# Performance work log

Hardware: AMD Instinct MI355X
Metric: run time of the kernel (lower is better)

The kernel has to match this reference:

```python
import jax, jax.numpy as jnp
import numpy as np

B, L, H, D_IN = 64, 4096, 128, 3

def setup_inputs() -> dict:
    key = jax.random.key(0)
    ks = jax.random.split(key, 9)
    def lin_w(k, fan_in, shape):
        bound = 1.0 / np.sqrt(fan_in)
        return jax.random.uniform(k, shape, jnp.float32, -bound, bound)
    return {
        "x": jax.random.normal(ks[0], (B, L, D_IN), jnp.float32),
        "Wp": lin_w(ks[1], D_IN, (D_IN, H)), "bp": lin_w(ks[2], D_IN, (H,)),
        "Wz": lin_w(ks[3], H, (H, H)),      "bz": lin_w(ks[4], H, (H,)),
        "Wh": lin_w(ks[5], H, (H, H)),      "bh": lin_w(ks[6], H, (H,)),
        "Wg": lin_w(ks[7], H, (H, 1)),      "bg": lin_w(ks[8], H, (1,)),
    }

def reference(x, Wp, bp, Wz, bz, Wh, bh, Wg, bg):
    # Batched projections across all timesteps (B, L, H)
    inp = x @ Wp + bp                      # input_proj
    z = jax.nn.sigmoid(inp @ Wz + bz)      # update gate
    h_tilde = jnp.tanh(inp @ Wh + bh)      # candidate
    # Linear recurrence h_t = a_t * h_{t-1} + b_t, h_{-1} = 0
    a = 1.0 - z
    b = z * h_tilde
    def combine(c1, c2):
        a1, b1 = c1
        a2, b2 = c2
        return (a1 * a2, b1 * a2 + b2)
    _, h = jax.lax.associative_scan(combine, (a, b), axis=1)  # h_t (since h_{-1}=0)
    # Readout uses h BEFORE the update at each step: preds_t = gauss_head(h_{t-1})
    h_prev = jnp.concatenate([jnp.zeros_like(h[:, :1]), h[:, :-1]], axis=1)
    preds = h_prev @ Wg + bg               # (B, L, 1)
    return preds
```

## Files before the change

### kernel.cpp

```cpp
#include <hip/hip_runtime.h>
#include <hip/hip_bf16.h>
#include <stdint.h>

#define B_   64
#define L_   4096
#define H_   128
#define HG_  32
#define NG_  4
#define TI_  256
#define NIT_ 16
#define PADI 136

typedef __attribute__((ext_vector_type(8))) short short8;
typedef __attribute__((ext_vector_type(4))) short short4v;
typedef __attribute__((ext_vector_type(4))) float floatx4;
typedef __attribute__((ext_vector_type(2))) float floatx2;

#define LOG2E 1.44269504088896340736f

__device__ __forceinline__ unsigned short f2bf(float f){
    unsigned int u = __float_as_uint(f);
    u += 0x7FFFu + ((u >> 16) & 1u);
    return (unsigned short)(u >> 16);
}
__device__ __forceinline__ float bf2f(unsigned short s){
    return __uint_as_float(((unsigned int)s) << 16);
}

__global__ void prep_w(const float* __restrict__ Wz, const float* __restrict__ Wh,
                       unsigned short* __restrict__ WzT, unsigned short* __restrict__ WhT){
    int b = blockIdx.x;
    const float* W = (b < 16) ? Wz : Wh;
    unsigned short* WT = (b < 16) ? WzT : WhT;
    int b16 = b & 15, tid = threadIdx.x;
    #pragma unroll
    for (int it = 0; it < 4; ++it){
        int idx = b16*1024 + it*256 + tid;
        int n = idx >> 7, k = idx & 127;
        WT[idx] = f2bf(W[k*H_ + n]);
    }
}

__global__ __launch_bounds__(1024, 4)
void fused_rnn(const float* __restrict__ x,
               const float* __restrict__ Wp, const float* __restrict__ bp,
               const float* __restrict__ bz, const float* __restrict__ bh,
               const float* __restrict__ Wg,
               const unsigned short* __restrict__ WzT,
               const unsigned short* __restrict__ WhT,
               float* __restrict__ partials)
{
    __shared__ __align__(16) unsigned short s_inp[TI_*PADI];
    __shared__ __align__(16) unsigned int  s_ab[TI_*HG_];
    __shared__ __align__(16) floatx2 s_agg[32*32];
    __shared__ float s_hh[32*32];

    const int bid = blockIdx.x;
    const int bb  = bid >> 2;
    const int g   = bid & 3;
    const int tid = threadIdx.x;
    const int wv = tid >> 6, lane = tid & 63, quad = lane >> 4, l15 = lane & 15;

    const int G   = wv >> 3;
    const int tt0 = wv & 7;
    const int sh  = tid & 31;
    const int ss  = tid >> 5;
    const int rh  = tid >> 5;
    const int rs  = tid & 31;
    const int cg  = tid & 31;
    const int tg  = tid >> 5;
    const int rt  = tid >> 2;
    const int rp  = tid & 3;

    const unsigned short* WT = G ? WhT : WzT;
    short8 bfr[2][4];
    #pragma unroll
    for (int ct = 0; ct < 2; ++ct)
        #pragma unroll
        for (int kk = 0; kk < 4; ++kk)
            bfr[ct][kk] = *(const short8*)&WT[(g*HG_ + ct*16 + l15)*H_ + kk*32 + quad*8];
    float biasv[2];
    #pragma unroll
    for (int ct = 0; ct < 2; ++ct)
        biasv[ct] = (G ? bh : bz)[g*HG_ + ct*16 + l15];
    const float wgv = Wg[g*HG_ + sh];
    float w0[4], w1[4], w2[4], bc[4];
    #pragma unroll
    for (int m = 0; m < 4; ++m){
        w0[m] = Wp[cg*4+m]; w1[m] = Wp[H_+cg*4+m]; w2[m] = Wp[2*H_+cg*4+m];
        bc[m] = bp[cg*4+m];
    }
    float h_run = 0.0f;

    for (int it = 0; it < NIT_; ++it){
        if (it > 0){
            float s = 0.0f;
            #pragma unroll
            for (int i = 0; i < 8; ++i){
                int col = rp*8 + i;
                s += ((const float*)s_ab)[rt*HG_ + (col ^ (rt & 31))];
            }
            s += __shfl_xor(s, 1);
            s += __shfl_xor(s, 2);
            if (rp == 0)
                partials[(((size_t)(g*B_ + bb)) << 12) + (it-1)*TI_ + rt] = s;
        }
        {
            const float* xr0 = x + ((size_t)bb*L_ + it*TI_ + tg*8)*3;
            #pragma unroll
            for (int j = 0; j < 8; ++j){
                int t = tg*8 + j;
                float x0 = xr0[j*3], x1 = xr0[j*3+1], x2 = xr0[j*3+2];
                short4v pk;
                #pragma unroll
                for (int m = 0; m < 4; ++m){
                    float v = bc[m];
                    v = fmaf(x0, w0[m], v);
                    v = fmaf(x1, w1[m], v);
                    v = fmaf(x2, w2[m], v);
                    pk[m] = (short)f2bf(v);
                }
                *(short4v*)&s_inp[t*PADI + cg*4] = pk;
            }
        }
        __syncthreads();

        #pragma unroll
        for (int tl = 0; tl < 2; ++tl){
            int tile = tt0 + tl*8;
            floatx4 acc0 = (floatx4){0.f,0.f,0.f,0.f};
            floatx4 acc1 = (floatx4){0.f,0.f,0.f,0.f};
            #pragma unroll
            for (int kk = 0; kk < 4; ++kk){
                short8 af = *(const short8*)&s_inp[(tile*16 + l15)*PADI + kk*32 + quad*8];
                acc0 = __builtin_amdgcn_mfma_f32_16x16x32_bf16(af, bfr[0][kk], acc0, 0, 0, 0);
                acc1 = __builtin_amdgcn_mfma_f32_16x16x32_bf16(af, bfr[1][kk], acc1, 0, 0, 0);
            }
            #pragma unroll
            for (int ct = 0; ct < 2; ++ct){
                floatx4 acc = ct ? acc1 : acc0;
                int hl = ct*16 + l15;
                #pragma unroll
                for (int e = 0; e < 4; ++e){
                    int t = tile*16 + quad*4 + e;
                    float v = acc[e] + biasv[ct];
                    float r;
                    if (G == 0){
                        r = __builtin_amdgcn_rcpf(1.0f + __builtin_amdgcn_exp2f(v * LOG2E));
                    } else {
                        float ex = __builtin_amdgcn_exp2f(2.0f*LOG2E*v);
                        r = 1.0f - 2.0f*__builtin_amdgcn_rcpf(ex + 1.0f);
                    }
                    ((unsigned short*)s_ab)[(t*HG_ + (hl ^ (t & 31)))*2 + G] = f2bf(r);
                }
            }
        }
        __syncthreads();

        float aj[8], bj[8];
        {
            float A = 1.0f, Q = 0.0f;
            #pragma unroll
            for (int j = 0; j < 8; ++j){
                int t = ss*8 + j;
                unsigned int u = s_ab[t*HG_ + (sh ^ (t & 31))];
                float a  = bf2f((unsigned short)(u & 0xffffu));
                float th = bf2f((unsigned short)(u >> 16));
                float b  = fmaf(-a, th, th);
                aj[j] = a; bj[j] = b;
                Q = fmaf(a, Q, b);
                A *= a;
            }
            s_agg[ss*32 + (sh ^ ss)] = (floatx2){A, Q};
        }
        __syncthreads();

        {
            floatx2 v = s_agg[rs*32 + (rh ^ rs)];
            float P = v[0], Hq = v[1];
            #pragma unroll
            for (int d = 1; d < 32; d <<= 1){
                float pP = __shfl_up(P, d, 32);
                float pH = __shfl_up(Hq, d, 32);
                if (rs >= d){
                    Hq = fmaf(P, pH, Hq);
                    P  = P * pP;
                }
            }
            float eP = __shfl_up(P, 1, 32);
            float eH = __shfl_up(Hq, 1, 32);
            if (rs == 0){ eP = 1.0f; eH = 0.0f; }
            float tP = __shfl(P, 31, 32);
            float tH = __shfl(Hq, 31, 32);
            s_hh[rs*32 + (rh ^ rs)] = fmaf(eP, h_run, eH);
            h_run = fmaf(tP, h_run, tH);
        }
        __syncthreads();

        {
            float hh = s_hh[ss*32 + (sh ^ ss)];
            #pragma unroll
            for (int j = 0; j < 8; ++j){
                int t = ss*8 + j;
                ((float*)s_ab)[t*HG_ + (sh ^ (t & 31))] = wgv * hh;
                hh = fmaf(aj[j], hh, bj[j]);
            }
        }
        __syncthreads();
    }

    {
        float s = 0.0f;
        #pragma unroll
        for (int i = 0; i < 8; ++i){
            int col = rp*8 + i;
            s += ((const float*)s_ab)[rt*HG_ + (col ^ (rt & 31))];
        }
        s += __shfl_xor(s, 1);
        s += __shfl_xor(s, 2);
        if (rp == 0)
            partials[(((size_t)(g*B_ + bb)) << 12) + (NIT_-1)*TI_ + rt] = s;
    }
}

__global__ __launch_bounds__(1024)
void gather(const float* __restrict__ partials, const float* __restrict__ bg,
            float* __restrict__ preds)
{
    size_t idx = (size_t)blockIdx.x*1024 + threadIdx.x;
    const size_t GSTRIDE = (size_t)B_ * L_;
    float s = bg[0];
    s += partials[idx];
    s += partials[GSTRIDE + idx];
    s += partials[2*GSTRIDE + idx];
    s += partials[3*GSTRIDE + idx];
    preds[idx] = s;
}

extern "C" void kernel_launch(void* const* d_in, const int* in_sizes, int n_in,
                              void* d_out, int out_size, void* d_ws, size_t ws_size,
                              hipStream_t stream){
    const float* x  = (const float*)d_in[0];
    const float* Wp = (const float*)d_in[1];
    const float* bp = (const float*)d_in[2];
    const float* Wz = (const float*)d_in[3];
    const float* bz = (const float*)d_in[4];
    const float* Wh = (const float*)d_in[5];
    const float* bh = (const float*)d_in[6];
    const float* Wg = (const float*)d_in[7];
    const float* bg = (const float*)d_in[8];
    float* preds = (float*)d_out;

    uint8_t* w8 = (uint8_t*)d_ws;
    unsigned short* WzT = (unsigned short*)(w8);
    unsigned short* WhT = (unsigned short*)(w8 + 32768);
    float* partials = (float*)(w8 + 65536);

    hipLaunchKernelGGL(prep_w, dim3(32), dim3(256), 0, stream, Wz, Wh, WzT, WhT);
    hipLaunchKernelGGL(fused_rnn, dim3(B_*NG_), dim3(1024), 0, stream,
                       x, Wp, bp, bz, bh, Wg, WzT, WhT, partials);
    hipLaunchKernelGGL(gather, dim3(B_*L_/1024), dim3(1024), 0, stream,
                       partials, bg, preds);
}
```

Measured before the change: 153.0 us.

## Fold weight prep into main kernel, prefetch x, and reduce readout via shuffles

```diff
diff --git a/kernel.cpp b/kernel.cpp
--- a/kernel.cpp
+++ b/kernel.cpp
@@ -10,9 +10,9 @@
 #define TI_  256
 #define NIT_ 16
 #define PADI 136
+#define SW(t) ((((t) << 2) ^ (t)) & 31)
 
 typedef __attribute__((ext_vector_type(8))) short short8;
-typedef __attribute__((ext_vector_type(4))) short short4v;
 typedef __attribute__((ext_vector_type(4))) float floatx4;
 typedef __attribute__((ext_vector_type(2))) float floatx2;
 
@@ -26,28 +26,17 @@
 __device__ __forceinline__ float bf2f(unsigned short s){
     return __uint_as_float(((unsigned int)s) << 16);
 }
-
-__global__ void prep_w(const float* __restrict__ Wz, const float* __restrict__ Wh,
-                       unsigned short* __restrict__ WzT, unsigned short* __restrict__ WhT){
-    int b = blockIdx.x;
-    const float* W = (b < 16) ? Wz : Wh;
-    unsigned short* WT = (b < 16) ? WzT : WhT;
-    int b16 = b & 15, tid = threadIdx.x;
-    #pragma unroll
-    for (int it = 0; it < 4; ++it){
-        int idx = b16*1024 + it*256 + tid;
-        int n = idx >> 7, k = idx & 127;
-        WT[idx] = f2bf(W[k*H_ + n]);
-    }
+__device__ __forceinline__ unsigned int pack2(float lo, float hi){
+    __hip_bfloat162 h = __float22bfloat162_rn(make_float2(lo, hi));
+    return *reinterpret_cast<unsigned int*>(&h);
 }
 
 __global__ __launch_bounds__(1024, 4)
 void fused_rnn(const float* __restrict__ x,
                const float* __restrict__ Wp, const float* __restrict__ bp,
-               const float* __restrict__ bz, const float* __restrict__ bh,
+               const float* __restrict__ Wz, const float* __restrict__ bz,
+               const float* __restrict__ Wh, const float* __restrict__ bh,
                const float* __restrict__ Wg,
-               const unsigned short* __restrict__ WzT,
-               const unsigned short* __restrict__ WhT,
                float* __restrict__ partials)
 {
     __shared__ __align__(16) unsigned short s_inp[TI_*PADI];
@@ -69,16 +58,34 @@
     const int rs  = tid & 31;
     const int cg  = tid & 31;
     const int tg  = tid >> 5;
-    const int rt  = tid >> 2;
-    const int rp  = tid & 3;
-
-    const unsigned short* WT = G ? WhT : WzT;
+
+    {
+        unsigned short* s_w = s_inp;
+        const int gate = tid >> 9;
+        const int r    = tid & 511;
+        const int k    = r >> 2;
+        const int nn0  = (r & 3) * 8;
+        const float* Wsrc = gate ? Wh : Wz;
+        const float* p = Wsrc + (size_t)k*H_ + g*HG_ + nn0;
+        floatx4 a = *(const floatx4*)p;
+        floatx4 b = *(const floatx4*)(p + 4);
+        #pragma unroll
+        for (int j = 0; j < 4; ++j){
+            s_w[gate*4096 + (nn0+j)*H_ + k]   = f2bf(a[j]);
+            s_w[gate*4096 + (nn0+4+j)*H_ + k] = f2bf(b[j]);
+        }
+    }
+    __syncthreads();
+
     short8 bfr[2][4];
-    #pragma unroll
-    for (int ct = 0; ct < 2; ++ct)
+    {
+        const unsigned short* wbase = s_inp + G*4096;
         #pragma unroll
-        for (int kk = 0; kk < 4; ++kk)
-            bfr[ct][kk] = *(const short8*)&WT[(g*HG_ + ct*16 + l15)*H_ + kk*32 + quad*8];
+        for (int ct = 0; ct < 2; ++ct)
+            #pragma unroll
+            for (int kk = 0; kk < 4; ++kk)
+                bfr[ct][kk] = *(const short8*)&wbase[(ct*16 + l15)*H_ + kk*32 + quad*8];
+    }
     float biasv[2];
     #pragma unroll
     for (int ct = 0; ct < 2; ++ct)
@@ -91,36 +98,36 @@
         bc[m] = bp[cg*4+m];
     }
     float h_run = 0.0f;
+    __syncthreads();
+
+    const float* xbase = x + ((size_t)bb*L_ + tg*8)*3;
+    floatx4 xr[6];
+    #pragma unroll
+    for (int q = 0; q < 6; ++q) xr[q] = *(const floatx4*)(xbase + q*4);
 
     for (int it = 0; it < NIT_; ++it){
-        if (it > 0){
-            float s = 0.0f;
-            #pragma unroll
-            for (int i = 0; i < 8; ++i){
-                int col = rp*8 + i;
-                s += ((const float*)s_ab)[rt*HG_ + (col ^ (rt & 31))];
-            }
-            s += __shfl_xor(s, 1);
-            s += __shfl_xor(s, 2);
-            if (rp == 0)
-                partials[(((size_t)(g*B_ + bb)) << 12) + (it-1)*TI_ + rt] = s;
-        }
-        {
-            const float* xr0 = x + ((size_t)bb*L_ + it*TI_ + tg*8)*3;
+        {
+            float xf[24];
+            #pragma unroll
+            for (int q = 0; q < 6; ++q){
+                xf[q*4+0] = xr[q][0]; xf[q*4+1] = xr[q][1];
+                xf[q*4+2] = xr[q][2]; xf[q*4+3] = xr[q][3];
+            }
+            if (it + 1 < NIT_){
+                const float* xn = xbase + (size_t)(it+1)*(TI_*3);
+                #pragma unroll
+                for (int q = 0; q < 6; ++q) xr[q] = *(const floatx4*)(xn + q*4);
+            }
             #pragma unroll
             for (int j = 0; j < 8; ++j){
                 int t = tg*8 + j;
-                float x0 = xr0[j*3], x1 = xr0[j*3+1], x2 = xr0[j*3+2];
-                short4v pk;
-                #pragma unroll
-                for (int m = 0; m < 4; ++m){
-                    float v = bc[m];
-                    v = fmaf(x0, w0[m], v);
-                    v = fmaf(x1, w1[m], v);
-                    v = fmaf(x2, w2[m], v);
-                    pk[m] = (short)f2bf(v);
-                }
-                *(short4v*)&s_inp[t*PADI + cg*4] = pk;
+                float x0 = xf[j*3], x1 = xf[j*3+1], x2 = xf[j*3+2];
+                float v0 = fmaf(x2, w2[0], fmaf(x1, w1[0], fmaf(x0, w0[0], bc[0])));
+                float v1 = fmaf(x2, w2[1], fmaf(x1, w1[1], fmaf(x0, w0[1], bc[1])));
+                float v2 = fmaf(x2, w2[2], fmaf(x1, w1[2], fmaf(x0, w0[2], bc[2])));
+                float v3 = fmaf(x2, w2[3], fmaf(x1, w1[3], fmaf(x0, w0[3], bc[3])));
+                uint2 st; st.x = pack2(v0, v1); st.y = pack2(v2, v3);
+                *(uint2*)&s_inp[t*PADI + cg*4] = st;
             }
         }
         __syncthreads();
@@ -151,7 +158,7 @@
                         float ex = __builtin_amdgcn_exp2f(2.0f*LOG2E*v);
                         r = 1.0f - 2.0f*__builtin_amdgcn_rcpf(ex + 1.0f);
                     }
-                    ((unsigned short*)s_ab)[(t*HG_ + (hl ^ (t & 31)))*2 + G] = f2bf(r);
+                    ((unsigned short*)s_ab)[(t*HG_ + (hl ^ SW(t)))*2 + G] = f2bf(r);
                 }
             }
         }
@@ -163,7 +170,7 @@
             #pragma unroll
             for (int j = 0; j < 8; ++j){
                 int t = ss*8 + j;
-                unsigned int u = s_ab[t*HG_ + (sh ^ (t & 31))];
+                unsigned int u = s_ab[t*HG_ + (sh ^ SW(t))];
                 float a  = bf2f((unsigned short)(u & 0xffffu));
                 float th = bf2f((unsigned short)(u >> 16));
                 float b  = fmaf(-a, th, th);
@@ -199,42 +206,36 @@
 
         {
             float hh = s_hh[ss*32 + (sh ^ ss)];
+            float y[8];
             #pragma unroll
             for (int j = 0; j < 8; ++j){
-                int t = ss*8 + j;
-                ((float*)s_ab)[t*HG_ + (sh ^ (t & 31))] = wgv * hh;
+                y[j] = wgv * hh;
                 hh = fmaf(aj[j], hh, bj[j]);
             }
-        }
-        __syncthreads();
-    }
-
-    {
-        float s = 0.0f;
-        #pragma unroll
-        for (int i = 0; i < 8; ++i){
-            int col = rp*8 + i;
-            s += ((const float*)s_ab)[rt*HG_ + (col ^ (rt & 31))];
-        }
-        s += __shfl_xor(s, 1);
-        s += __shfl_xor(s, 2);
-        if (rp == 0)
-            partials[(((size_t)(g*B_ + bb)) << 12) + (NIT_-1)*TI_ + rt] = s;
+            #pragma unroll
+            for (int d = 16; d >= 1; d >>= 1)
+                #pragma unroll
+                for (int j = 0; j < 8; ++j)
+                    y[j] += __shfl_xor(y[j], d, 32);
+            if (sh == 0){
+                float* dst = partials + (size_t)(g*B_ + bb)*L_ + it*TI_ + ss*8;
+                *(floatx4*)dst     = (floatx4){y[0], y[1], y[2], y[3]};
+                *(floatx4*)(dst+4) = (floatx4){y[4], y[5], y[6], y[7]};
+            }
+        }
     }
 }
 
 __global__ __launch_bounds__(1024)
-void gather(const float* __restrict__ partials, const float* __restrict__ bg,
-            float* __restrict__ preds)
+void gather(const floatx4* __restrict__ partials, const float* __restrict__ bg,
+            floatx4* __restrict__ preds)
 {
-    size_t idx = (size_t)blockIdx.x*1024 + threadIdx.x;
-    const size_t GSTRIDE = (size_t)B_ * L_;
-    float s = bg[0];
-    s += partials[idx];
-    s += partials[GSTRIDE + idx];
-    s += partials[2*GSTRIDE + idx];
-    s += partials[3*GSTRIDE + idx];
-    preds[idx] = s;
+    size_t i = (size_t)blockIdx.x*1024 + threadIdx.x;
+    const size_t S = (size_t)B_ * L_ / 4;
+    float b = bg[0];
+    floatx4 v = partials[i] + partials[S+i] + partials[2*S+i] + partials[3*S+i];
+    v[0] += b; v[1] += b; v[2] += b; v[3] += b;
+    preds[i] = v;
 }
 
 extern "C" void kernel_launch(void* const* d_in, const int* in_sizes, int n_in,
@@ -252,13 +253,10 @@
     float* preds = (float*)d_out;
 
     uint8_t* w8 = (uint8_t*)d_ws;
-    unsigned short* WzT = (unsigned short*)(w8);
-    unsigned short* WhT = (unsigned short*)(w8 + 32768);
-    float* partials = (float*)(w8 + 65536);
-
-    hipLaunchKernelGGL(prep_w, dim3(32), dim3(256), 0, stream, Wz, Wh, WzT, WhT);
+    float* partials = (float*)w8;
+
     hipLaunchKernelGGL(fused_rnn, dim3(B_*NG_), dim3(1024), 0, stream,
-                       x, Wp, bp, bz, bh, Wg, WzT, WhT, partials);
-    hipLaunchKernelGGL(gather, dim3(B_*L_/1024), dim3(1024), 0, stream,
-                       partials, bg, preds);
-}
+                       x, Wp, bp, Wz, bz, Wh, bh, Wg, partials);
+    hipLaunchKernelGGL(gather, dim3(B_*L_/4096), dim3(1024), 0, stream,
+                       (const floatx4*)partials, bg, (floatx4*)preds);
+}
```

Result: slower. 193.2 us (+26.3%).
